# Optimization experiments

Hardware: AMD Instinct MI355X
Metric: run time of the kernel (lower is better)

## Reference

```python
import jax, jax.numpy as jnp
import numpy as np

B, S, D, H = 2, 4096, 1024, 16
DH = D // H  # 64


def setup_inputs() -> dict:
    key = jax.random.key(0)
    ks = jax.random.split(key, 5)
    x = jax.random.normal(ks[0], (B, S, D), dtype=jnp.float32)
    scale = 1.0 / np.sqrt(D)
    Wq = jax.random.normal(ks[1], (D, D), dtype=jnp.float32) * scale
    Wk = jax.random.normal(ks[2], (D, D), dtype=jnp.float32) * scale
    Wv = jax.random.normal(ks[3], (D, D), dtype=jnp.float32) * scale
    Wo = jax.random.normal(ks[4], (D, D), dtype=jnp.float32) * scale
    bo = jnp.zeros((D,), dtype=jnp.float32)
    return {"x": x, "Wq": Wq, "Wk": Wk, "Wv": Wv, "Wo": Wo, "bo": bo}


def reference(x, Wq, Wk, Wv, Wo, bo):
    b, s, d = x.shape
    # QKV projections (no bias), split heads: [b, s, H, DH]
    q = (x @ Wq).reshape(b, s, H, DH)
    k = (x @ Wk).reshape(b, s, H, DH)
    v = (x @ Wv).reshape(b, s, H, DH)
    # scores: [b, H, s, s]
    scores = jnp.einsum("bqhd,bkhd->bhqk", q, k)
    # causal mask: upper triangle (j > i) set to -inf, then scale by sqrt(d_head)
    causal = jnp.triu(jnp.ones((s, s), dtype=bool), k=1)
    scores = jnp.where(causal, -jnp.inf, scores)
    weights = jax.nn.softmax(scores / jnp.sqrt(jnp.float32(DH)), axis=-1)
    # dropout rate is 0.0 -> identity
    ctx = jnp.einsum("bhqk,bkhd->bqhd", weights, v).reshape(b, s, d)
    return ctx @ Wo + bo
```

## Files before the change

### kernel.cpp

```cpp
#include <hip/hip_runtime.h>
#include <hip/hip_bf16.h>
#include <stdint.h>
#include <math.h>

#define BATCH 2
#define S_LEN 4096
#define DMODEL 1024
#define NH 16
#define DHEAD 64
#define MTOK (BATCH * S_LEN)

#define QSCALE 0.1803368801111793f

typedef unsigned short u16;
typedef __attribute__((ext_vector_type(8))) short bf16x8;
typedef __attribute__((ext_vector_type(4))) float f32x4;
typedef __attribute__((ext_vector_type(16))) float f32x16;
typedef __attribute__((ext_vector_type(4))) unsigned short u16x4;

__device__ __forceinline__ float b2f(u16 u) {
  union { unsigned int i; float f; } v; v.i = ((unsigned int)u) << 16; return v.f;
}
__device__ __forceinline__ u16 f2b(float f) {
  union { float f; unsigned int i; } v; v.f = f;
  unsigned int r = v.i + 0x7FFF + ((v.i >> 16) & 1);
  return (u16)(r >> 16);
}
__device__ __forceinline__ unsigned int pk2(float hi, float lo) {
  union { float f; unsigned int u; } a, b; a.f = hi; b.f = lo;
  return __builtin_amdgcn_perm(a.u, b.u, 0x07060302u);
}
__device__ __forceinline__ void pswap(unsigned int& a, unsigned int& b) {
  asm("v_permlane32_swap_b32 %0, %1" : "+v"(a), "+v"(b));
}

__device__ __forceinline__ void gl_lds16(const u16* g, u16* l) {
  __builtin_amdgcn_global_load_lds(
      (__attribute__((address_space(1))) void*)(u16*)g,
      (__attribute__((address_space(3))) void*)l, 16, 0, 0);
}

__global__ void detect_dtype(const unsigned int* __restrict__ x, int* __restrict__ flag) {
  __shared__ int cnt;
  if (threadIdx.x == 0) cnt = 0;
  __syncthreads();
  int c = 0;
  for (int i = threadIdx.x; i < 4096; i += 256) {
    unsigned int w = x[i];
    int e = (w >> 7) & 0xFF;
    if (e >= 100 && e <= 135) c++;
  }
  atomicAdd(&cnt, c);
  __syncthreads();
  if (threadIdx.x == 0) *flag = (cnt > 2048) ? 1 : 0;
}

__global__ void convert_x(const void* __restrict__ xin, u16* __restrict__ xc,
                          const int* __restrict__ flagp) {
  const int isb = *flagp;
  long e = ((long)blockIdx.x * 256 + threadIdx.x) * 4;
  if (isb) {
    *(uint2*)&xc[e] = *(const uint2*)((const u16*)xin + e);
  } else {
    float4 f = *(const float4*)((const float*)xin + e);
    xc[e + 0] = f2b(f.x);
    xc[e + 1] = f2b(f.y);
    xc[e + 2] = f2b(f.z);
    xc[e + 3] = f2b(f.w);
  }
}

__global__ void transpose4(const void* __restrict__ W0, const void* __restrict__ W1,
                           const void* __restrict__ W2, const void* __restrict__ W3,
                           u16* __restrict__ out, const int* __restrict__ flagp) {
  __shared__ u16 tile[32][33];
  const int isb = *flagp;
  int z = blockIdx.z;
  const void* W = (z == 0) ? W0 : (z == 1) ? W1 : (z == 2) ? W2 : W3;
  u16* o = out + (long)z * (DMODEL * DMODEL);
  int x = blockIdx.x * 32 + threadIdx.x;
  int y0 = blockIdx.y * 32;
  if (isb) {
    const u16* Wb = (const u16*)W;
#pragma unroll
    for (int i = 0; i < 32; i += 8)
      tile[threadIdx.y + i][threadIdx.x] = Wb[(long)(y0 + threadIdx.y + i) * DMODEL + x];
  } else {
    const float* Wf = (const float*)W;
#pragma unroll
    for (int i = 0; i < 32; i += 8)
      tile[threadIdx.y + i][threadIdx.x] = f2b(Wf[(long)(y0 + threadIdx.y + i) * DMODEL + x]);
  }
  __syncthreads();
  int x2 = blockIdx.y * 32 + threadIdx.x;
  int y2 = blockIdx.x * 32;
#pragma unroll
  for (int i = 0; i < 32; i += 8)
    o[(long)(y2 + threadIdx.y + i) * DMODEL + x2] = tile[threadIdx.x][threadIdx.y + i];
}

#define BM3 128
#define BN3 256
#define BK3 32
#define NT3 (DMODEL / BK3)
#define BUF3 12288

#define VM6 asm volatile("s_waitcnt vmcnt(6)" ::: "memory")
#define VM0 asm volatile("s_waitcnt vmcnt(0)" ::: "memory")
#define BARX do { asm volatile("" ::: "memory"); __builtin_amdgcn_s_barrier(); \
                  asm volatile("" ::: "memory"); } while (0)

#define STAGE3(t_, dst_)                                                          \
  do {                                                                            \
    const u16* a_ = pA + (t_) * BK3;                                              \
    const u16* b_ = pB + (t_) * BK3;                                              \
    u16* ad_ = (dst_) + w * 1024;                                                 \
    u16* bd_ = (dst_) + 4096 + w * 2048;                                          \
    gl_lds16(a_, ad_);                                                            \
    gl_lds16(a_ + 16 * DMODEL, ad_ + 512);                                        \
    gl_lds16(b_, bd_);                                                            \
    gl_lds16(b_ + 16 * DMODEL, bd_ + 512);                                        \
    gl_lds16(b_ + 32 * DMODEL, bd_ + 1024);                                       \
    gl_lds16(b_ + 48 * DMODEL, bd_ + 1536);                                       \
  } while (0)

#define GEMM_CORE3(A_, Bt_)                                                       \
  __shared__ __align__(16) u16 lds[2 * BUF3];                                     \
  const int tid = threadIdx.x;                                                    \
  const int w = tid >> 6;                                                         \
  const int lane = tid & 63;                                                      \
  const int m0 = blockIdx.y * BM3;                                                \
  const int n0 = blockIdx.x * BN3;                                                \
  const int wn = w * 64;                                                          \
  const int lc = lane & 15;                                                       \
  const int lq = lane >> 4;                                                       \
  const u16* pA = (A_) + (long)(m0 + w * 32 + (lane >> 2)) * DMODEL + (lane & 3) * 8; \
  const u16* pB = (Bt_) + (long)(n0 + w * 64 + (lane >> 2)) * DMODEL + (lane & 3) * 8; \
  f32x4 acc[8][4] = {};                                                           \
  STAGE3(0, lds);                                                                 \
  STAGE3(1, lds + BUF3);                                                          \
  for (int t = 0; t < NT3; ++t) {                                                 \
    if (t < NT3 - 1) { VM6; } else { VM0; }                                       \
    BARX;                                                                         \
    const u16* la = lds + (t & 1) * BUF3;                                         \
    const u16* lb = la + 4096;                                                    \
    bf16x8 af[8], bg[4];                                                          \
    _Pragma("unroll")                                                             \
    for (int j = 0; j < 4; ++j)                                                   \
      bg[j] = *(const bf16x8*)&lb[(wn + j * 16 + lc) * 32 + lq * 8];              \
    _Pragma("unroll")                                                             \
    for (int i = 0; i < 8; ++i)                                                   \
      af[i] = *(const bf16x8*)&la[(i * 16 + lc) * 32 + lq * 8];                   \
    _Pragma("unroll")                                                             \
    for (int i = 0; i < 8; ++i)                                                   \
      _Pragma("unroll")                                                           \
      for (int j = 0; j < 4; ++j)                                                 \
        acc[i][j] = __builtin_amdgcn_mfma_f32_16x16x32_bf16(af[i], bg[j], acc[i][j], 0, 0, 0); \
    BARX;                                                                         \
    if (t + 2 < NT3) { STAGE3(t + 2, lds + (t & 1) * BUF3); }                     \
  }

__global__ __launch_bounds__(256, 2)
void gemm_qkv(const u16* __restrict__ A, const u16* __restrict__ Bt,
              u16* __restrict__ Qo, u16* __restrict__ Ko, u16* __restrict__ Vo) {
  GEMM_CORE3(A, Bt)
#pragma unroll
  for (int i = 0; i < 8; ++i) {
#pragma unroll
    for (int j = 0; j < 4; ++j) {
      int n = n0 + wn + j * 16 + lc;
      int rgn = n >> 10;
      int nn = n & 1023;
      int h = nn >> 6, dh = nn & (DHEAD - 1);
      int m_base = m0 + i * 16 + lq * 4;
      int b = m_base >> 12, s0q = m_base & (S_LEN - 1);
      if (rgn == 2) {
        long idx_v = (((long)(b * NH + h)) * DHEAD + dh) * S_LEN + s0q;
        u16x4 vv;
#pragma unroll
        for (int r = 0; r < 4; ++r) vv[r] = f2b(acc[i][j][r]);
        *(u16x4*)&Vo[idx_v] = vv;
      } else {
        float sc = (rgn == 0) ? QSCALE : 1.0f;
        u16* dst = (rgn == 0) ? Qo : Ko;
#pragma unroll
        for (int r = 0; r < 4; ++r) {
          long idx_r = (((long)(b * NH + h)) * S_LEN + s0q + r) * DHEAD + dh;
          dst[idx_r] = f2b(acc[i][j][r] * sc);
        }
      }
    }
  }
}

__global__ __launch_bounds__(256, 2)
void gemm_out(const u16* __restrict__ A, const u16* __restrict__ Bt,
              const void* __restrict__ bias, void* __restrict__ C,
              const int* __restrict__ flagp) {
  GEMM_CORE3(A, Bt)
  const int isb = *flagp;
#pragma unroll
  for (int i = 0; i < 8; ++i) {
#pragma unroll
    for (int j = 0; j < 4; ++j) {
      int n = n0 + wn + j * 16 + lc;
      float bv = isb ? b2f(((const u16*)bias)[n]) : ((const float*)bias)[n];
#pragma unroll
      for (int r = 0; r < 4; ++r) {
        int m = m0 + i * 16 + lq * 4 + r;
        float v = acc[i][j][r] + bv;
        if (isb) ((u16*)C)[(long)m * DMODEL + n] = f2b(v);
        else     ((float*)C)[(long)m * DMODEL + n] = v;
      }
    }
  }
}

__global__ __launch_bounds__(256, 2)
void flash_attn(const u16* __restrict__ Q, const u16* __restrict__ K,
                const u16* __restrict__ Vt, u16* __restrict__ ctx) {
  __shared__ __align__(16) u16 lK[64 * 64];
  __shared__ __align__(16) u16 lV[64 * 64];

  const int tid = threadIdx.x;
  const int w = tid >> 6;
  const int lane = tid & 63;
  const int l31 = lane & 31;
  const int l5 = lane >> 5;

  const int hb = blockIdx.x;
  const int h = hb & (NH - 1);
  const int b = hb >> 4;
  const int qt = gridDim.y - 1 - (int)blockIdx.y;
  const int q0 = qt * 128;

  const int bh = b * NH + h;
  const u16* Qb = Q + (long)bh * S_LEN * DHEAD;
  const u16* Kb = K + (long)bh * S_LEN * DHEAD;
  const u16* Vb = Vt + (long)bh * DHEAD * S_LEN;

  const int qa = q0 + w * 32;
  const int myq = qa + l31;

  bf16x8 aq[4];
#pragma unroll
  for (int c = 0; c < 4; ++c)
    aq[c] = *(const bf16x8*)(Qb + (long)myq * DHEAD + c * 16 + l5 * 8);

  union OU { unsigned int wd[4]; bf16x8 v; } ones;
#pragma unroll
  for (int i = 0; i < 4; ++i) ones.wd[i] = 0x3F803F80u;

  const int srow = tid >> 2;
  const int sc0 = (tid & 3) * 2;
  const int sd0 = srow * 64 + ((sc0 ^ (srow & 7)) * 8);
  const int sd1 = srow * 64 + (((sc0 + 1) ^ (srow & 7)) * 8);
  const u16* kp = Kb + (long)srow * DHEAD + sc0 * 8;
  const u16* vp = Vb + (long)srow * S_LEN + sc0 * 8;

  const int kmax = q0 + 64;
  bf16x8 kr0 = *(const bf16x8*)kp;
  bf16x8 kr1 = *(const bf16x8*)(kp + 8);
  bf16x8 vr0 = *(const bf16x8*)vp;
  bf16x8 vr1 = *(const bf16x8*)(vp + 8);
  const u16* kpre = kp + 64 * DHEAD;
  const u16* vpre = vp + 64;

  f32x16 o0 = {}, o1 = {};
  f32x16 lacc = {};
  const int xsw = l31 & 7;

  int offK[4][2], offV[4][2];
#pragma unroll
  for (int c = 0; c < 4; ++c) {
    const int ch = c * 2 + l5;
    offK[c][0] = l31 * 64 + ((ch ^ xsw) * 8);
    offK[c][1] = (32 + l31) * 64 + ((ch ^ xsw) * 8);
    offV[c][0] = offK[c][0];
    offV[c][1] = offK[c][1];
  }

  for (int k0 = 0; k0 <= kmax; k0 += 64) {
    *(bf16x8*)&lK[sd0] = kr0;
    *(bf16x8*)&lK[sd1] = kr1;
    *(bf16x8*)&lV[sd0] = vr0;
    *(bf16x8*)&lV[sd1] = vr1;
    __syncthreads();

    if (k0 + 64 <= kmax) {
      kr0 = *(const bf16x8*)kpre;
      kr1 = *(const bf16x8*)(kpre + 8);
      vr0 = *(const bf16x8*)vpre;
      vr1 = *(const bf16x8*)(vpre + 8);
      kpre += 64 * DHEAD;
      vpre += 64;
    }

    if (k0 <= qa + 31) {
      f32x16 s0 = {}, s1 = {};
      __builtin_amdgcn_s_setprio(1);
#pragma unroll
      for (int c = 0; c < 4; ++c) {
        bf16x8 ak0 = *(const bf16x8*)&lK[offK[c][0]];
        bf16x8 ak1 = *(const bf16x8*)&lK[offK[c][1]];
        s0 = __builtin_amdgcn_mfma_f32_32x32x16_bf16(ak0, aq[c], s0, 0, 0, 0);
        s1 = __builtin_amdgcn_mfma_f32_32x32x16_bf16(ak1, aq[c], s1, 0, 0, 0);
      }
      __builtin_amdgcn_s_setprio(0);

      const bool masked = (k0 + 63 > qa);
      union BPU { unsigned int wd[4]; bf16x8 v; };
      BPU bp[4];
#pragma unroll
      for (int ph = 0; ph < 2; ++ph) {
        const f32x16 sv = ph ? s1 : s0;
        float p[16];
#pragma unroll
        for (int rr = 0; rr < 16; ++rr) {
          float e = __builtin_amdgcn_exp2f(sv[rr]);
          if (masked) {
            int kv = k0 + ph * 32 + (rr & 3) + 8 * (rr >> 2) + 4 * l5;
            e = (kv > myq) ? 0.0f : e;
          }
          p[rr] = e;
        }
#pragma unroll
        for (int g = 0; g < 2; ++g) {
          unsigned int A0 = pk2(p[8 * g + 1], p[8 * g + 0]);
          unsigned int A1 = pk2(p[8 * g + 3], p[8 * g + 2]);
          unsigned int B0 = pk2(p[8 * g + 5], p[8 * g + 4]);
          unsigned int B1 = pk2(p[8 * g + 7], p[8 * g + 6]);
          pswap(A0, B0);
          pswap(A1, B1);
          const int kc = ph * 2 + g;
          bp[kc].wd[0] = A0; bp[kc].wd[1] = A1;
          bp[kc].wd[2] = B0; bp[kc].wd[3] = B1;
        }
      }

      __builtin_amdgcn_s_setprio(1);
#pragma unroll
      for (int kc = 0; kc < 4; ++kc) {
        bf16x8 av0 = *(const bf16x8*)&lV[offV[kc][0]];
        bf16x8 av1 = *(const bf16x8*)&lV[offV[kc][1]];
        o0 = __builtin_amdgcn_mfma_f32_32x32x16_bf16(av0, bp[kc].v, o0, 0, 0, 0);
        o1 = __builtin_amdgcn_mfma_f32_32x32x16_bf16(av1, bp[kc].v, o1, 0, 0, 0);
        lacc = __builtin_amdgcn_mfma_f32_32x32x16_bf16(ones.v, bp[kc].v, lacc, 0, 0, 0);
      }
      __builtin_amdgcn_s_setprio(0);
    }
    __syncthreads();
  }

  float inv = 1.0f / lacc[0];

  u16* cp = ctx + ((long)(b * S_LEN + myq)) * DMODEL + h * DHEAD;
#pragma unroll
  for (int d32 = 0; d32 < 2; ++d32) {
    const f32x16 ov = d32 ? o1 : o0;
#pragma unroll
    for (int g = 0; g < 4; ++g) {
      u16x4 st;
#pragma unroll
      for (int r = 0; r < 4; ++r) st[r] = f2b(ov[4 * g + r] * inv);
      *(u16x4*)&cp[d32 * 32 + g * 8 + l5 * 4] = st;
    }
  }
}

extern "C" void kernel_launch(void* const* d_in, const int* in_sizes, int n_in,
                              void* d_out, int out_size, void* d_ws, size_t ws_size,
                              hipStream_t stream) {
  const void* x  = d_in[0];
  const void* Wq = d_in[1];
  const void* Wk = d_in[2];
  const void* Wv = d_in[3];
  const void* Wo = d_in[4];
  const void* bo = d_in[5];
  u16* ws = (u16*)d_ws;

  u16* wt  = ws;
  u16* wto = wt + 3145728;
  u16* Qb  = ws + 4194304;
  u16* Vtb = ws + 12582912;
  u16* xc  = ws + 20971520;
  u16* ctx = xc;
  int* flag = (int*)(ws + 29360128);
  u16* Kb  = (u16*)d_out;

  detect_dtype<<<1, 256, 0, stream>>>((const unsigned int*)x, flag);
  convert_x<<<8192, 256, 0, stream>>>(x, xc, flag);
  transpose4<<<dim3(32, 32, 4), dim3(32, 8), 0, stream>>>(Wq, Wk, Wv, Wo, wt, flag);

  gemm_qkv<<<dim3(3 * DMODEL / BN3, MTOK / BM3), 256, 0, stream>>>(xc, wt, Qb, Kb, Vtb);

  flash_attn<<<dim3(NH * BATCH, S_LEN / 128), 256, 0, stream>>>(Qb, Kb, Vtb, ctx);

  gemm_out<<<dim3(DMODEL / BN3, MTOK / BM3), 256, 0, stream>>>(ctx, wto, bo, d_out, flag);
}
```

Measured before the change: 288.9 us.

## Enlarge GEMM tiles to 256x256 with 8 waves, 4-stage pipeline and block swizzle

Both projection GEMMs now use 256x256 output tiles computed by 512-thread workgroups (8 waves in a 2x4 arrangement). Global-to-LDS staging moves to a 4-buffer ring with three tiles in flight, which drops one of the two barriers per k-step. The flat grid is swizzled for L2 locality, and MFMA issue gets raised wave priority. This aims to raise operand reuse and hide load latency, at the cost of 128KB of LDS per block and fewer blocks (384 and 128), which risks poor occupancy and load balance on the smaller output GEMM.

```diff
diff --git a/kernel.cpp b/kernel.cpp
--- a/kernel.cpp
+++ b/kernel.cpp
@@ -99,80 +99,82 @@
     o[(long)(y2 + threadIdx.y + i) * DMODEL + x2] = tile[threadIdx.x][threadIdx.y + i];
 }
 
-#define BM3 128
-#define BN3 256
-#define BK3 32
-#define NT3 (DMODEL / BK3)
-#define BUF3 12288
-
-#define VM6 asm volatile("s_waitcnt vmcnt(6)" ::: "memory")
+#define BKX 32
+#define NTX (DMODEL / BKX)
+#define BUFX 16384
+
+#define VM8 asm volatile("s_waitcnt vmcnt(8)" ::: "memory")
+#define VM4 asm volatile("s_waitcnt vmcnt(4)" ::: "memory")
 #define VM0 asm volatile("s_waitcnt vmcnt(0)" ::: "memory")
 #define BARX do { asm volatile("" ::: "memory"); __builtin_amdgcn_s_barrier(); \
                   asm volatile("" ::: "memory"); } while (0)
 
-#define STAGE3(t_, dst_)                                                          \
+#define STAGE4(t_, b_)                                                            \
   do {                                                                            \
-    const u16* a_ = pA + (t_) * BK3;                                              \
-    const u16* b_ = pB + (t_) * BK3;                                              \
-    u16* ad_ = (dst_) + w * 1024;                                                 \
-    u16* bd_ = (dst_) + 4096 + w * 2048;                                          \
-    gl_lds16(a_, ad_);                                                            \
-    gl_lds16(a_ + 16 * DMODEL, ad_ + 512);                                        \
-    gl_lds16(b_, bd_);                                                            \
-    gl_lds16(b_ + 16 * DMODEL, bd_ + 512);                                        \
-    gl_lds16(b_ + 32 * DMODEL, bd_ + 1024);                                       \
-    gl_lds16(b_ + 48 * DMODEL, bd_ + 1536);                                       \
+    const u16* a_ = pA + (t_) * BKX;                                              \
+    const u16* bt_ = pB + (t_) * BKX;                                             \
+    u16* d_ = lds + (b_) * BUFX + w * 512;                                        \
+    gl_lds16(a_, d_);                                                             \
+    gl_lds16(a_ + 128 * DMODEL, d_ + 4096);                                       \
+    gl_lds16(bt_, d_ + 8192);                                                     \
+    gl_lds16(bt_ + 128 * DMODEL, d_ + 12288);                                     \
   } while (0)
 
-#define GEMM_CORE3(A_, Bt_)                                                       \
-  __shared__ __align__(16) u16 lds[2 * BUF3];                                     \
+#define GEMM_CORE4(A_, Bt_, NX_)                                                  \
+  __shared__ __align__(16) u16 lds[4 * BUFX];                                     \
   const int tid = threadIdx.x;                                                    \
   const int w = tid >> 6;                                                         \
   const int lane = tid & 63;                                                      \
-  const int m0 = blockIdx.y * BM3;                                                \
-  const int n0 = blockIdx.x * BN3;                                                \
-  const int wn = w * 64;                                                          \
+  const int nwg = (int)gridDim.x;                                                 \
+  const int wg = (int)blockIdx.x;                                                 \
+  const int swz = (wg & 7) * (nwg >> 3) + (wg >> 3);                              \
+  const int m0 = (swz / (NX_)) * 256;                                             \
+  const int n0 = (swz % (NX_)) * 256;                                             \
+  const int wr = w >> 2;                                                          \
+  const int wc = w & 3;                                                           \
   const int lc = lane & 15;                                                       \
   const int lq = lane >> 4;                                                       \
-  const u16* pA = (A_) + (long)(m0 + w * 32 + (lane >> 2)) * DMODEL + (lane & 3) * 8; \
-  const u16* pB = (Bt_) + (long)(n0 + w * 64 + (lane >> 2)) * DMODEL + (lane & 3) * 8; \
+  const u16* pA = (A_) + (long)(m0 + w * 16 + (lane >> 2)) * DMODEL + (lane & 3) * 8; \
+  const u16* pB = (Bt_) + (long)(n0 + w * 16 + (lane >> 2)) * DMODEL + (lane & 3) * 8; \
   f32x4 acc[8][4] = {};                                                           \
-  STAGE3(0, lds);                                                                 \
-  STAGE3(1, lds + BUF3);                                                          \
-  for (int t = 0; t < NT3; ++t) {                                                 \
-    if (t < NT3 - 1) { VM6; } else { VM0; }                                       \
+  STAGE4(0, 0);                                                                   \
+  STAGE4(1, 1);                                                                   \
+  STAGE4(2, 2);                                                                   \
+  for (int t = 0; t < NTX; ++t) {                                                 \
+    if (t < NTX - 2) { VM8; } else if (t == NTX - 2) { VM4; } else { VM0; }       \
     BARX;                                                                         \
-    const u16* la = lds + (t & 1) * BUF3;                                         \
-    const u16* lb = la + 4096;                                                    \
+    if (t + 3 < NTX) STAGE4(t + 3, (t + 3) & 3);                                  \
+    const u16* la = lds + (t & 3) * BUFX;                                         \
+    const u16* lb = la + 8192;                                                    \
     bf16x8 af[8], bg[4];                                                          \
     _Pragma("unroll")                                                             \
     for (int j = 0; j < 4; ++j)                                                   \
-      bg[j] = *(const bf16x8*)&lb[(wn + j * 16 + lc) * 32 + lq * 8];              \
+      bg[j] = *(const bf16x8*)&lb[(wc * 64 + j * 16 + lc) * 32 + lq * 8];         \
     _Pragma("unroll")                                                             \
     for (int i = 0; i < 8; ++i)                                                   \
-      af[i] = *(const bf16x8*)&la[(i * 16 + lc) * 32 + lq * 8];                   \
+      af[i] = *(const bf16x8*)&la[(wr * 128 + i * 16 + lc) * 32 + lq * 8];        \
+    __builtin_amdgcn_s_setprio(1);                                                \
     _Pragma("unroll")                                                             \
     for (int i = 0; i < 8; ++i)                                                   \
       _Pragma("unroll")                                                           \
       for (int j = 0; j < 4; ++j)                                                 \
         acc[i][j] = __builtin_amdgcn_mfma_f32_16x16x32_bf16(af[i], bg[j], acc[i][j], 0, 0, 0); \
-    BARX;                                                                         \
-    if (t + 2 < NT3) { STAGE3(t + 2, lds + (t & 1) * BUF3); }                     \
-  }
-
-__global__ __launch_bounds__(256, 2)
+    __builtin_amdgcn_s_setprio(0);                                                \
+  }
+
+__global__ __launch_bounds__(512, 2)
 void gemm_qkv(const u16* __restrict__ A, const u16* __restrict__ Bt,
               u16* __restrict__ Qo, u16* __restrict__ Ko, u16* __restrict__ Vo) {
-  GEMM_CORE3(A, Bt)
+  GEMM_CORE4(A, Bt, 12)
 #pragma unroll
   for (int i = 0; i < 8; ++i) {
 #pragma unroll
     for (int j = 0; j < 4; ++j) {
-      int n = n0 + wn + j * 16 + lc;
+      int n = n0 + wc * 64 + j * 16 + lc;
       int rgn = n >> 10;
       int nn = n & 1023;
       int h = nn >> 6, dh = nn & (DHEAD - 1);
-      int m_base = m0 + i * 16 + lq * 4;
+      int m_base = m0 + wr * 128 + i * 16 + lq * 4;
       int b = m_base >> 12, s0q = m_base & (S_LEN - 1);
       if (rgn == 2) {
         long idx_v = (((long)(b * NH + h)) * DHEAD + dh) * S_LEN + s0q;
@@ -193,21 +195,21 @@
   }
 }
 
-__global__ __launch_bounds__(256, 2)
+__global__ __launch_bounds__(512, 2)
 void gemm_out(const u16* __restrict__ A, const u16* __restrict__ Bt,
               const void* __restrict__ bias, void* __restrict__ C,
               const int* __restrict__ flagp) {
-  GEMM_CORE3(A, Bt)
+  GEMM_CORE4(A, Bt, 4)
   const int isb = *flagp;
 #pragma unroll
   for (int i = 0; i < 8; ++i) {
 #pragma unroll
     for (int j = 0; j < 4; ++j) {
-      int n = n0 + wn + j * 16 + lc;
+      int n = n0 + wc * 64 + j * 16 + lc;
       float bv = isb ? b2f(((const u16*)bias)[n]) : ((const float*)bias)[n];
 #pragma unroll
       for (int r = 0; r < 4; ++r) {
-        int m = m0 + i * 16 + lq * 4 + r;
+        int m = m0 + wr * 128 + i * 16 + lq * 4 + r;
         float v = acc[i][j][r] + bv;
         if (isb) ((u16*)C)[(long)m * DMODEL + n] = f2b(v);
         else     ((float*)C)[(long)m * DMODEL + n] = v;
@@ -392,9 +394,9 @@
   convert_x<<<8192, 256, 0, stream>>>(x, xc, flag);
   transpose4<<<dim3(32, 32, 4), dim3(32, 8), 0, stream>>>(Wq, Wk, Wv, Wo, wt, flag);
 
-  gemm_qkv<<<dim3(3 * DMODEL / BN3, MTOK / BM3), 256, 0, stream>>>(xc, wt, Qb, Kb, Vtb);
+  gemm_qkv<<<dim3(12 * 32), 512, 0, stream>>>(xc, wt, Qb, Kb, Vtb);
 
   flash_attn<<<dim3(NH * BATCH, S_LEN / 128), 256, 0, stream>>>(Qb, Kb, Vtb, ctx);
 
-  gemm_out<<<dim3(DMODEL / BN3, MTOK / BM3), 256, 0, stream>>>(ctx, wto, bo, d_out, flag);
-}
+  gemm_out<<<dim3(4 * 32), 512, 0, stream>>>(ctx, wto, bo, d_out, flag);
+}
```

Result: slower. 316.8 us (+9.6%).
